# Kernel optimization log

Measured on AMD Instinct MI355X. Metric: run time of the kernel, lower is better.

The kernel has to match this reference:

```python
import jax, jax.numpy as jnp
import numpy as np

LN_EPS = 1e-5

def _ln(x, g, b):
    m = x.mean(-1, keepdims=True)
    v = jnp.mean((x - m) ** 2, axis=-1, keepdims=True)
    return (x - m) * jax.lax.rsqrt(v + LN_EPS) * g + b


def setup_inputs() -> dict:
    key = jax.random.key(0)
    ks = jax.random.split(key, 8)
    B, S, H = 8, 4096, 2048
    V, L, E = 32, 8, 64   # vocab_size, symbol seq_len, embedding_dim
    sc = 0.02
    d = {}
    d["hidden_states"] = jax.random.normal(ks[0], (B, S, H), jnp.float32)
    # uniform in (0,1) for Gumbel noise: g = -log(-log(u))
    d["gumbel_u"] = jax.random.uniform(ks[1], (B, L, V), jnp.float32, 1e-6, 1.0 - 1e-6)
    d["enc_w1"] = jax.random.normal(ks[2], (256, H), jnp.float32) * sc
    d["enc_b1"] = jnp.zeros((256,), jnp.float32)
    d["ln1_g"] = jnp.ones((256,), jnp.float32)
    d["ln1_b"] = jnp.zeros((256,), jnp.float32)
    d["enc_w2"] = jax.random.normal(ks[3], (L * V, 256), jnp.float32) * sc
    d["enc_b2"] = jnp.zeros((L * V,), jnp.float32)
    d["embed"] = jax.random.normal(ks[4], (V, E), jnp.float32) * sc
    d["dec_w1"] = jax.random.normal(ks[5], (256, L * E), jnp.float32) * sc
    d["dec_b1"] = jnp.zeros((256,), jnp.float32)
    d["ln2_g"] = jnp.ones((256,), jnp.float32)
    d["ln2_b"] = jnp.zeros((256,), jnp.float32)
    d["dec_w2"] = jax.random.normal(ks[6], (H, 256), jnp.float32) * sc
    d["dec_b2"] = jnp.zeros((H,), jnp.float32)
    return d


def reference(hidden_states, gumbel_u, enc_w1, enc_b1, ln1_g, ln1_b, enc_w2, enc_b2,
              embed, dec_w1, dec_b1, ln2_g, ln2_b, dec_w2, dec_b2):
    V, L, TAU = 32, 8, 1.0
    B, S, H = hidden_states.shape
    E = embed.shape[1]
    # encode: mean-pool over sequence, then MLP -> logits [B, L, V]
    pooled = hidden_states.mean(axis=1)
    h = _ln(pooled @ enc_w1.T + enc_b1, ln1_g, ln1_b)
    h = jax.nn.gelu(h, approximate=False)
    logits = (h @ enc_w2.T + enc_b2).reshape(B, L, V)
    # gumbel-softmax with straight-through (hard) estimator
    g = -jnp.log(-jnp.log(gumbel_u))
    y_soft = jax.nn.softmax((logits + g) / TAU, axis=-1)
    idx = jnp.argmax(y_soft, axis=-1)
    y_hard = jax.nn.one_hot(idx, V, dtype=y_soft.dtype)
    soft_symbols = y_hard - jax.lax.stop_gradient(y_soft) + y_soft
    # decode: embed symbols, flatten, MLP back to hidden size
    emb = jnp.einsum('blv,ve->ble', soft_symbols, embed).reshape(B, L * E)
    dh = _ln(emb @ dec_w1.T + dec_b1, ln2_g, ln2_b)
    dh = jax.nn.gelu(dh, approximate=False)
    decoded = dh @ dec_w2.T + dec_b2            # [B, H]
    # residual + 0.1 * broadcast over sequence
    return hidden_states + 0.1 * decoded[:, None, :]
```

## Files before the change

### kernel.cpp

```cpp
#include <hip/hip_runtime.h>
#include <math.h>

#define B 8
#define S 4096
#define H 2048
#define LSYM 8
#define EMB 64
#define SPLIT 64
#define CHUNK (S / SPLIT)

typedef float f32x4 __attribute__((ext_vector_type(4)));

__global__ __launch_bounds__(256) void pool_partial(const float* __restrict__ hid,
                                                    float* __restrict__ part) {
    const int sp = blockIdx.x;
    const int b  = blockIdx.y;
    const int t  = threadIdx.x;
    const float* slab = hid + (size_t)b * S * H + (size_t)sp * CHUNK * H;
    const int iters = CHUNK * (H / 1024);
    f32x4 a[8];
#pragma unroll
    for (int k = 0; k < 8; ++k) a[k] = (f32x4)(0.f);
    for (int i = 0; i < iters; i += 8) {
#pragma unroll
        for (int k = 0; k < 8; ++k) {
            const f32x4 v = *reinterpret_cast<const f32x4*>(slab + (size_t)(i + k) * 1024 + t * 4);
            a[k] += v;
        }
    }
    const f32x4 e = a[0] + a[2] + a[4] + a[6];
    const f32x4 o = a[1] + a[3] + a[5] + a[7];
    float* dst = part + ((size_t)sp * B + b) * H;
    *reinterpret_cast<f32x4*>(dst + t * 4)        = e;
    *reinterpret_cast<f32x4*>(dst + 1024 + t * 4) = o;
}

__global__ __launch_bounds__(256) void pool_reduce(const float* __restrict__ part,
                                                   float* __restrict__ pooled) {
    const int i4 = blockIdx.x * 256 + threadIdx.x;
    if (i4 >= B * H / 4) return;
    float4 acc = {0.f, 0.f, 0.f, 0.f};
    for (int sp = 0; sp < SPLIT; ++sp) {
        const float4 v = *reinterpret_cast<const float4*>(part + (size_t)sp * B * H + (size_t)i4 * 4);
        acc.x += v.x; acc.y += v.y; acc.z += v.z; acc.w += v.w;
    }
    const float inv = 1.0f / (float)S;
    acc.x *= inv; acc.y *= inv; acc.z *= inv; acc.w *= inv;
    *reinterpret_cast<float4*>(pooled + (size_t)i4 * 4) = acc;
}

__global__ __launch_bounds__(256) void enc1_matvec(const float* __restrict__ pooled,
                                                   const float* __restrict__ ew1,
                                                   const float* __restrict__ eb1,
                                                   float* __restrict__ out1) {
    const int wv   = (blockIdx.x * 256 + threadIdx.x) >> 6;
    const int lane = threadIdx.x & 63;
    const int b = wv >> 8, t = wv & 255;
    const float4* wrow = reinterpret_cast<const float4*>(ew1 + (size_t)t * H);
    const float4* prow = reinterpret_cast<const float4*>(pooled + b * H);
    float acc = 0.f;
#pragma unroll
    for (int i = 0; i < 8; ++i) {
        const float4 w = wrow[lane + 64 * i];
        const float4 p = prow[lane + 64 * i];
        acc += w.x * p.x + w.y * p.y + w.z * p.z + w.w * p.w;
    }
    for (int off = 32; off; off >>= 1) acc += __shfl_xor(acc, off, 64);
    if (lane == 0) out1[b * 256 + t] = acc + eb1[t];
}

__device__ __forceinline__ float block_sum256(float x, float* red) {
    const int t = threadIdx.x;
    red[t] = x;
    __syncthreads();
    for (int s = 128; s > 0; s >>= 1) {
        if (t < s) red[t] += red[t + s];
        __syncthreads();
    }
    const float r = red[0];
    __syncthreads();
    return r;
}

__global__ __launch_bounds__(256) void mlp_middle(
    const float* __restrict__ out1, const float* __restrict__ gu,
    const float* __restrict__ g1,  const float* __restrict__ bb1,
    const float* __restrict__ ew2, const float* __restrict__ eb2,
    const float* __restrict__ emb_tab,
    const float* __restrict__ dw1, const float* __restrict__ db1,
    const float* __restrict__ g2,  const float* __restrict__ bb2,
    float* __restrict__ hs2) {
    __shared__ float red[256];
    __shared__ float hs[256];
    __shared__ float es[LSYM * EMB];

    const int b = blockIdx.x;
    const int t = threadIdx.x;

    float acc = out1[b * 256 + t];
    {
        const float m = block_sum256(acc, red) * (1.0f / 256.0f);
        const float d = acc - m;
        const float v = block_sum256(d * d, red) * (1.0f / 256.0f);
        float x = d * rsqrtf(v + 1e-5f) * g1[t] + bb1[t];
        x = 0.5f * x * (1.0f + erff(x * 0.70710678118654752f));
        hs[t] = x;
    }
    __syncthreads();

    float z;
    {
        float a2 = eb2[t];
        const float* w2row = ew2 + t * 256;
        for (int k = 0; k < 256; k += 4) {
            const float4 w = *reinterpret_cast<const float4*>(w2row + k);
            a2 += w.x * hs[k] + w.y * hs[k + 1] + w.z * hs[k + 2] + w.w * hs[k + 3];
        }
        const float u = gu[b * 256 + t];
        z = a2 - logf(-logf(u));
    }

    {
        int   bi = t & 31;
        float bz = z;
        for (int off = 16; off; off >>= 1) {
            const float oz = __shfl_xor(bz, off, 32);
            const int   oi = __shfl_xor(bi, off, 32);
            if (oz > bz || (oz == bz && oi < bi)) { bz = oz; bi = oi; }
        }
        const int l = t >> 5, v32 = t & 31;
        es[l * EMB + v32]      = emb_tab[bi * EMB + v32];
        es[l * EMB + 32 + v32] = emb_tab[bi * EMB + 32 + v32];
    }
    __syncthreads();

    float a3 = db1[t];
    {
        const float* d1row = dw1 + t * (LSYM * EMB);
        for (int k = 0; k < LSYM * EMB; k += 4) {
            const float4 w = *reinterpret_cast<const float4*>(d1row + k);
            a3 += w.x * es[k] + w.y * es[k + 1] + w.z * es[k + 2] + w.w * es[k + 3];
        }
    }
    {
        const float m2 = block_sum256(a3, red) * (1.0f / 256.0f);
        const float dd = a3 - m2;
        const float vv = block_sum256(dd * dd, red) * (1.0f / 256.0f);
        float y = dd * rsqrtf(vv + 1e-5f) * g2[t] + bb2[t];
        y = 0.5f * y * (1.0f + erff(y * 0.70710678118654752f));
        hs2[b * 256 + t] = y;
    }
}

__global__ __launch_bounds__(256) void dec2_matvec(const float* __restrict__ hs2,
                                                   const float* __restrict__ dw2,
                                                   const float* __restrict__ db2,
                                                   float* __restrict__ dec_sc) {
    const int wv   = (blockIdx.x * 256 + threadIdx.x) >> 6;
    const int lane = threadIdx.x & 63;
    const int b = wv >> 11, j = wv & 2047;
    const float4 w = reinterpret_cast<const float4*>(dw2 + (size_t)j * 256)[lane];
    const float4 h = reinterpret_cast<const float4*>(hs2 + b * 256)[lane];
    float acc = w.x * h.x + w.y * h.y + w.z * h.z + w.w * h.w;
    for (int off = 32; off; off >>= 1) acc += __shfl_xor(acc, off, 64);
    if (lane == 0) dec_sc[b * 2048 + j] = 0.1f * (acc + db2[j]);
}

__global__ __launch_bounds__(256) void residual_add(const float* __restrict__ hid,
                                                    const float* __restrict__ dec,
                                                    float* __restrict__ out) {
    const size_t tid0 = (size_t)blockIdx.x * 256 + threadIdx.x;
    const int h4 = (int)(tid0 & (H / 4 - 1));
    const f32x4* __restrict__ hv4 = reinterpret_cast<const f32x4*>(hid);
    const float4* __restrict__ dv4 = reinterpret_cast<const float4*>(dec);
    f32x4* __restrict__ ov4 = reinterpret_cast<f32x4*>(out);
    size_t i = tid0;
#pragma unroll
    for (int b = 0; b < B; ++b) {
        const float4 dv = dv4[b * (H / 4) + h4];
        const f32x4 dvv = {dv.x, dv.y, dv.z, dv.w};
#pragma unroll
        for (int r = 0; r < 2; ++r, i += (size_t)1 << 20) {
            const f32x4 hv = hv4[i];
            const f32x4 o = hv + dvv;
            __builtin_nontemporal_store(o, &ov4[i]);
        }
    }
}

extern "C" void kernel_launch(void* const* d_in, const int* in_sizes, int n_in,
                              void* d_out, int out_size, void* d_ws, size_t ws_size,
                              hipStream_t stream) {
    const float* hid   = (const float*)d_in[0];
    const float* gu    = (const float*)d_in[1];
    const float* ew1   = (const float*)d_in[2];
    const float* eb1   = (const float*)d_in[3];
    const float* g1    = (const float*)d_in[4];
    const float* bb1   = (const float*)d_in[5];
    const float* ew2   = (const float*)d_in[6];
    const float* eb2   = (const float*)d_in[7];
    const float* emb   = (const float*)d_in[8];
    const float* dw1   = (const float*)d_in[9];
    const float* db1   = (const float*)d_in[10];
    const float* g2    = (const float*)d_in[11];
    const float* bb2   = (const float*)d_in[12];
    const float* dw2   = (const float*)d_in[13];
    const float* db2   = (const float*)d_in[14];
    float* out = (float*)d_out;

    float* part   = (float*)d_ws;
    float* pooled = part + (size_t)SPLIT * B * H;
    float* dec_sc = pooled + (size_t)B * H;
    float* out1   = dec_sc + (size_t)B * H;
    float* hs2    = out1 + (size_t)B * 256;

    pool_partial<<<dim3(SPLIT, B), 256, 0, stream>>>(hid, part);
    pool_reduce<<<(B * H / 4 + 255) / 256, 256, 0, stream>>>(part, pooled);
    enc1_matvec<<<B * 256 / 4, 256, 0, stream>>>(pooled, ew1, eb1, out1);
    mlp_middle<<<B, 256, 0, stream>>>(out1, gu, g1, bb1, ew2, eb2, emb,
                                      dw1, db1, g2, bb2, hs2);
    dec2_matvec<<<B * 2048 / 4, 256, 0, stream>>>(hs2, dw2, db2, dec_sc);
    residual_add<<<4096, 256, 0, stream>>>(hid, dec_sc, out);
}
```

Baseline: 179.6 us.

## Fuse pool reduction and encoder MLP stages via last-block atomic counters

Merges the pooling reduce into the partial-pool kernel and the middle MLP into the first encoder matvec, using a per-batch atomic counter so the last block of each group does the follow-on reduction. This removes two kernel launches and their inter-kernel gaps. It relies on a workspace counter region that is never zeroed and instead uses modulo arithmetic on the running count. The final reduction runs on only one block per batch, which serializes that tail work.

```diff
diff --git a/kernel.cpp b/kernel.cpp
--- a/kernel.cpp
+++ b/kernel.cpp
@@ -11,8 +11,10 @@
 
 typedef float f32x4 __attribute__((ext_vector_type(4)));
 
-__global__ __launch_bounds__(256) void pool_partial(const float* __restrict__ hid,
-                                                    float* __restrict__ part) {
+__global__ __launch_bounds__(256) void pool_partial_fused(const float* __restrict__ hid,
+                                                          float* __restrict__ part,
+                                                          float* __restrict__ pooled,
+                                                          unsigned int* __restrict__ cnt) {
     const int sp = blockIdx.x;
     const int b  = blockIdx.y;
     const int t  = threadIdx.x;
@@ -33,40 +35,30 @@
     float* dst = part + ((size_t)sp * B + b) * H;
     *reinterpret_cast<f32x4*>(dst + t * 4)        = e;
     *reinterpret_cast<f32x4*>(dst + 1024 + t * 4) = o;
-}
-
-__global__ __launch_bounds__(256) void pool_reduce(const float* __restrict__ part,
-                                                   float* __restrict__ pooled) {
-    const int i4 = blockIdx.x * 256 + threadIdx.x;
-    if (i4 >= B * H / 4) return;
-    float4 acc = {0.f, 0.f, 0.f, 0.f};
-    for (int sp = 0; sp < SPLIT; ++sp) {
-        const float4 v = *reinterpret_cast<const float4*>(part + (size_t)sp * B * H + (size_t)i4 * 4);
-        acc.x += v.x; acc.y += v.y; acc.z += v.z; acc.w += v.w;
+
+    __syncthreads();
+    __threadfence();
+    __shared__ int is_last;
+    if (t == 0) {
+        const unsigned int old = __hip_atomic_fetch_add(&cnt[b * 32], 1u,
+                                   __ATOMIC_ACQ_REL, __HIP_MEMORY_SCOPE_AGENT);
+        is_last = ((old & (SPLIT - 1)) == (SPLIT - 1)) ? 1 : 0;
+    }
+    __syncthreads();
+    if (!is_last) return;
+    __threadfence();
+
+    const f32x4* pp = reinterpret_cast<const f32x4*>(part);
+    f32x4 acc0 = (f32x4)(0.f), acc1 = (f32x4)(0.f);
+    for (int s2 = 0; s2 < SPLIT; ++s2) {
+        const size_t base = ((size_t)s2 * B + b) * (H / 4);
+        acc0 += pp[base + t];
+        acc1 += pp[base + t + 256];
     }
     const float inv = 1.0f / (float)S;
-    acc.x *= inv; acc.y *= inv; acc.z *= inv; acc.w *= inv;
-    *reinterpret_cast<float4*>(pooled + (size_t)i4 * 4) = acc;
-}
-
-__global__ __launch_bounds__(256) void enc1_matvec(const float* __restrict__ pooled,
-                                                   const float* __restrict__ ew1,
-                                                   const float* __restrict__ eb1,
-                                                   float* __restrict__ out1) {
-    const int wv   = (blockIdx.x * 256 + threadIdx.x) >> 6;
-    const int lane = threadIdx.x & 63;
-    const int b = wv >> 8, t = wv & 255;
-    const float4* wrow = reinterpret_cast<const float4*>(ew1 + (size_t)t * H);
-    const float4* prow = reinterpret_cast<const float4*>(pooled + b * H);
-    float acc = 0.f;
-#pragma unroll
-    for (int i = 0; i < 8; ++i) {
-        const float4 w = wrow[lane + 64 * i];
-        const float4 p = prow[lane + 64 * i];
-        acc += w.x * p.x + w.y * p.y + w.z * p.z + w.w * p.w;
-    }
-    for (int off = 32; off; off >>= 1) acc += __shfl_xor(acc, off, 64);
-    if (lane == 0) out1[b * 256 + t] = acc + eb1[t];
+    acc0 *= inv; acc1 *= inv;
+    reinterpret_cast<f32x4*>(pooled + (size_t)b * H)[t]       = acc0;
+    reinterpret_cast<f32x4*>(pooled + (size_t)b * H)[t + 256] = acc1;
 }
 
 __device__ __forceinline__ float block_sum256(float x, float* red) {
@@ -82,21 +74,56 @@
     return r;
 }
 
-__global__ __launch_bounds__(256) void mlp_middle(
-    const float* __restrict__ out1, const float* __restrict__ gu,
+__global__ __launch_bounds__(256) void enc1_fused(
+    const float* __restrict__ pooled,
+    const float* __restrict__ ew1, const float* __restrict__ eb1,
+    float* __restrict__ out1,
+    const float* __restrict__ gu,
     const float* __restrict__ g1,  const float* __restrict__ bb1,
     const float* __restrict__ ew2, const float* __restrict__ eb2,
     const float* __restrict__ emb_tab,
     const float* __restrict__ dw1, const float* __restrict__ db1,
     const float* __restrict__ g2,  const float* __restrict__ bb2,
-    float* __restrict__ hs2) {
+    float* __restrict__ hs2,
+    unsigned int* __restrict__ cnt) {
     __shared__ float red[256];
-    __shared__ float hs[256];
+    __shared__ float hsm[256];
     __shared__ float es[LSYM * EMB];
 
-    const int b = blockIdx.x;
-    const int t = threadIdx.x;
-
+    const int bid = blockIdx.x;
+    const int t   = threadIdx.x;
+    const int wv  = t >> 6, lane = t & 63;
+    const int bb  = bid >> 6;
+
+    {
+        const int o  = bid * 4 + wv;
+        const int tt = o & 255;
+        const float4* wrow = reinterpret_cast<const float4*>(ew1 + (size_t)tt * H);
+        const float4* prow = reinterpret_cast<const float4*>(pooled + bb * H);
+        float acc = 0.f;
+#pragma unroll
+        for (int i = 0; i < 8; ++i) {
+            const float4 w = wrow[lane + 64 * i];
+            const float4 p = prow[lane + 64 * i];
+            acc += w.x * p.x + w.y * p.y + w.z * p.z + w.w * p.w;
+        }
+        for (int off = 32; off; off >>= 1) acc += __shfl_xor(acc, off, 64);
+        if (lane == 0) out1[o] = acc + eb1[tt];
+    }
+
+    __syncthreads();
+    __threadfence();
+    __shared__ int is_last;
+    if (t == 0) {
+        const unsigned int old = __hip_atomic_fetch_add(&cnt[(8 + bb) * 32], 1u,
+                                   __ATOMIC_ACQ_REL, __HIP_MEMORY_SCOPE_AGENT);
+        is_last = ((old & 63u) == 63u) ? 1 : 0;
+    }
+    __syncthreads();
+    if (!is_last) return;
+    __threadfence();
+
+    const int b = bb;
     float acc = out1[b * 256 + t];
     {
         const float m = block_sum256(acc, red) * (1.0f / 256.0f);
@@ -104,23 +131,19 @@
         const float v = block_sum256(d * d, red) * (1.0f / 256.0f);
         float x = d * rsqrtf(v + 1e-5f) * g1[t] + bb1[t];
         x = 0.5f * x * (1.0f + erff(x * 0.70710678118654752f));
-        hs[t] = x;
-    }
-    __syncthreads();
-
-    float z;
+        hsm[t] = x;
+    }
+    __syncthreads();
+
     {
         float a2 = eb2[t];
         const float* w2row = ew2 + t * 256;
         for (int k = 0; k < 256; k += 4) {
             const float4 w = *reinterpret_cast<const float4*>(w2row + k);
-            a2 += w.x * hs[k] + w.y * hs[k + 1] + w.z * hs[k + 2] + w.w * hs[k + 3];
+            a2 += w.x * hsm[k] + w.y * hsm[k + 1] + w.z * hsm[k + 2] + w.w * hsm[k + 3];
         }
         const float u = gu[b * 256 + t];
-        z = a2 - logf(-logf(u));
-    }
-
-    {
+        const float z = a2 - logf(-logf(u));
         int   bi = t & 31;
         float bz = z;
         for (int off = 16; off; off >>= 1) {
@@ -213,12 +236,11 @@
     float* dec_sc = pooled + (size_t)B * H;
     float* out1   = dec_sc + (size_t)B * H;
     float* hs2    = out1 + (size_t)B * 256;
-
-    pool_partial<<<dim3(SPLIT, B), 256, 0, stream>>>(hid, part);
-    pool_reduce<<<(B * H / 4 + 255) / 256, 256, 0, stream>>>(part, pooled);
-    enc1_matvec<<<B * 256 / 4, 256, 0, stream>>>(pooled, ew1, eb1, out1);
-    mlp_middle<<<B, 256, 0, stream>>>(out1, gu, g1, bb1, ew2, eb2, emb,
-                                      dw1, db1, g2, bb2, hs2);
+    unsigned int* cnt = (unsigned int*)(hs2 + (size_t)B * 256);
+
+    pool_partial_fused<<<dim3(SPLIT, B), 256, 0, stream>>>(hid, part, pooled, cnt);
+    enc1_fused<<<512, 256, 0, stream>>>(pooled, ew1, eb1, out1, gu, g1, bb1, ew2, eb2,
+                                        emb, dw1, db1, g2, bb2, hs2, cnt);
     dec2_matvec<<<B * 2048 / 4, 256, 0, stream>>>(hs2, dw2, db2, dec_sc);
     residual_add<<<4096, 256, 0, stream>>>(hid, dec_sc, out);
 }
```

New measurement: 271.2 us. 51.0% more time.
